# Optimization experiments

Measured on AMD Instinct MI355X. Metric: run time of the kernel, lower is better.

## Reference

```python
import jax, jax.numpy as jnp
import numpy as np

NUM_HEADS = 16
LORA_RANK = 64
LORA_ALPHA = 1.0


def setup_inputs() -> dict:
    key = jax.random.key(0)
    ks = jax.random.split(key, 9)
    B, N, C, r = 16, 1024, 1024, LORA_RANK
    s = lambda k, shp, sc=0.02: (jax.random.normal(k, shp, dtype=jnp.float32) * sc)
    return {
        "x": jax.random.normal(ks[0], (B, N, C), dtype=jnp.float32),
        "W_qkv": s(ks[1], (3 * C, C)),
        "b_qkv": s(ks[2], (3 * C,)),
        "lora_kA": s(ks[3], (r, C), 1.0 / np.sqrt(r)),
        "lora_kB": s(ks[4], (C, r)),
        "lora_vA": s(ks[5], (r, C), 1.0 / np.sqrt(r)),
        "lora_vB": s(ks[6], (C, r)),
        "W_proj": s(ks[7], (C, C)),
        "b_proj": s(ks[8], (C,)),
    }


def reference(x, W_qkv, b_qkv, lora_kA, lora_kB, lora_vA, lora_vB, W_proj, b_proj):
    B, N, C = x.shape
    H = NUM_HEADS
    D = C // H
    scale = D ** -0.5
    lora_scale = LORA_ALPHA / LORA_RANK

    # qkv projection: (B,N,3C)
    qkv = x @ W_qkv.T + b_qkv
    # LoRA deltas for k and v: x @ A.T @ B.T * (alpha/rank)
    k_lora = ((x @ lora_kA.T) @ lora_kB.T) * lora_scale  # (B,N,C)
    v_lora = ((x @ lora_vA.T) @ lora_vB.T) * lora_scale  # (B,N,C)

    qkv = qkv.reshape(B, N, 3, H, D).transpose(2, 0, 3, 1, 4)  # (3,B,H,N,D)
    q, k, v = qkv[0], qkv[1], qkv[2]
    k = k + k_lora.reshape(B, N, H, D).transpose(0, 2, 1, 3)
    v = v + v_lora.reshape(B, N, H, D).transpose(0, 2, 1, 3)

    attn = jnp.einsum('bhqd,bhkd->bhqk', q, k) * scale  # (B,H,N,N)
    attn = jax.nn.softmax(attn, axis=-1)
    out = jnp.einsum('bhqk,bhkd->bhqd', attn, v)  # (B,H,N,D)
    out = out.transpose(0, 2, 1, 3).reshape(B, N, C)
    return out @ W_proj.T + b_proj
```

## Files before the change

kernel.cpp:

```cpp
#include <hip/hip_runtime.h>
#include <hip/hip_bf16.h>
#include <stdint.h>

#define B_  16
#define N_  1024
#define C_  1024
#define H_  16
#define Dh  64
#define M_  (B_*N_)
#define QSCALE (0.125f * 1.44269504f)

typedef __attribute__((ext_vector_type(8)))  short short8;
typedef __attribute__((ext_vector_type(4)))  float f32x4;
typedef __attribute__((ext_vector_type(16))) float f32x16;

__device__ __forceinline__ ushort f2bf(float f) {
  union { float f; uint32_t u; } v; v.f = f;
  uint32_t u = v.u;
  u += 0x7fffu + ((u >> 16) & 1u);
  return (ushort)(u >> 16);
}

__device__ __forceinline__ float exp2fast(float x) {
#if __has_builtin(__builtin_amdgcn_exp2f)
  return __builtin_amdgcn_exp2f(x);
#else
  return exp2f(x);
#endif
}

__device__ __forceinline__ uint32_t pkbf(float lo, float hi) {
  float2 f; f.x = lo; f.y = hi;
  union { __hip_bfloat162 b; uint32_t u; } c;
  c.b = __float22bfloat162_rn(f);
  return c.u;
}

__device__ __forceinline__ void gload_lds16(const ushort* g, ushort* l) {
  __builtin_amdgcn_global_load_lds((const __attribute__((address_space(1))) void*)g,
                                   (__attribute__((address_space(3))) void*)l, 16, 0, 0);
}

struct CastSegs {
  const float* src[7];
  ushort*      dst[7];
  int          cum[7];
  float        scale[7];
};

__global__ void cast_all_k(CastSegs sg, int total4) {
  int i = blockIdx.x * blockDim.x + threadIdx.x;
  int stride = gridDim.x * blockDim.x;
  for (; i < total4; i += stride) {
    int s = 0;
    #pragma unroll
    for (int k = 0; k < 6; ++k) s += (i >= sg.cum[k]);
    int base = s ? sg.cum[s-1] : 0;
    int li = i - base;
    float sc = sg.scale[s];
    float4 v = reinterpret_cast<const float4*>(sg.src[s])[li];
    ushort4 o;
    o.x = f2bf(v.x * sc);
    o.y = f2bf(v.y * sc);
    o.z = f2bf(v.z * sc);
    o.w = f2bf(v.w * sc);
    reinterpret_cast<ushort4*>(sg.dst[s])[li] = o;
  }
}

template<int MODE>
__global__ __launch_bounds__(256)
void gemm128(const ushort* __restrict__ A, int lda,
             const ushort* __restrict__ Bm, int ldb,
             const float* __restrict__ bias,
             const ushort* __restrict__ A2,
             const ushort* __restrict__ B2k, const ushort* __restrict__ B2v,
             ushort* __restrict__ oq, ushort* __restrict__ ok, ushort* __restrict__ ov,
             float* __restrict__ of, int ldo)
{
  __shared__ ushort sA[2][128*32];
  __shared__ ushort sB[2][128*32];
  const int t = threadIdx.x;
  const int lane = t & 63, w = t >> 6;
  const int wr = w >> 1, wc = w & 1;
  const int r = lane & 15, g = lane >> 4;
  const int m0 = blockIdx.x * 128, n0 = blockIdx.y * 128;

  const int s = n0 >> 10;
  int nt = 32;
  const ushort* A2b = nullptr; const ushort* B2 = nullptr; int n0loc = 0;
  if (MODE == 1 && s == 1) {
    nt = 34;
    A2b = A2;
    B2 = B2k;
    n0loc = n0 - 1024;
  }
  if (MODE == 3) nt = 34;

  auto stage = [&](int buf, int tt) {
    const ushort* Ab; const ushort* Bb; int ldaT, ldbT;
    if (tt < 32) { Ab = A + m0*lda + tt*32; ldaT = lda; Bb = Bm + n0*ldb + tt*32; ldbT = ldb; }
    else if (MODE == 3) {
      Ab = A2 + m0*64 + (tt-32)*32; ldaT = 64;
      Bb = B2k + n0*128 + (tt-32)*32; ldbT = 128;
    } else {
      Ab = A2b + m0*128 + (tt-32)*32; ldaT = 128;
      Bb = B2 + n0loc*64 + (tt-32)*32; ldbT = 64;
    }
    #pragma unroll
    for (int i = 0; i < 2; ++i) {
      int c = i*256 + t;
      gload_lds16(Ab + (c>>2)*ldaT + (c&3)*8, &sA[buf][c*8]);
      gload_lds16(Bb + (c>>2)*ldbT + (c&3)*8, &sB[buf][c*8]);
    }
  };

  f32x4 acc[4][4];
  #pragma unroll
  for (int i=0;i<4;++i)
    #pragma unroll
    for (int j=0;j<4;++j) acc[i][j] = (f32x4){0.f,0.f,0.f,0.f};

  stage(0, 0);
  __syncthreads();
  for (int tt = 0; tt < nt; ++tt) {
    int cur = tt & 1;
    if (tt + 1 < nt) stage(cur ^ 1, tt + 1);
    short8 af[4], bfr[4];
    #pragma unroll
    for (int i=0;i<4;++i) af[i]  = *(const short8*)&sA[cur][(wr*64 + i*16 + r)*32 + g*8];
    #pragma unroll
    for (int j=0;j<4;++j) bfr[j] = *(const short8*)&sB[cur][(wc*64 + j*16 + r)*32 + g*8];
    #pragma unroll
    for (int i=0;i<4;++i)
      #pragma unroll
      for (int j=0;j<4;++j)
        acc[i][j] = __builtin_amdgcn_mfma_f32_16x16x32_bf16(af[i], bfr[j], acc[i][j], 0,0,0);
    __syncthreads();
  }

  #pragma unroll
  for (int i=0;i<4;++i) {
    #pragma unroll
    for (int j=0;j<4;++j) {
      #pragma unroll
      for (int rr=0;rr<4;++rr) {
        int m = m0 + wr*64 + i*16 + g*4 + rr;
        int n = n0 + wc*64 + j*16 + r;
        float v = acc[i][j][rr];
        if (MODE == 0) {
          oq[m*128 + n] = f2bf(v);
        } else if (MODE == 1) {
          v += bias[n];
          int b = m >> 10, nq = m & 1023;
          int c = n & 1023, h = c >> 6, d = c & 63;
          int idx = ((b*H_ + h)*N_ + nq)*Dh + d;
          if (s == 0)      oq[idx] = f2bf(v * QSCALE);
          else             ok[idx] = f2bf(v);
        } else if (MODE == 3) {
          v += bias[m];
          int h = m >> 6, d = m & 63;
          int b = n >> 10, nq = n & 1023;
          ov[((b*H_ + h)*Dh + d)*N_ + nq] = f2bf(v);
        } else {
          of[m*ldo + n] = v + bias[n];
        }
      }
    }
  }
}

__global__ __launch_bounds__(256, 4)
void flash_attn32(const ushort* __restrict__ qb, const ushort* __restrict__ kb,
                  const ushort* __restrict__ vb, ushort* __restrict__ out)
{
  __shared__ ushort Kt[2][64*64];
  __shared__ ushort Vt[2][64*64];
  const int t = threadIdx.x, w = t >> 6, lane = t & 63;
  const int ql = lane & 31, hi = lane >> 5;

  int bid = (blockIdx.x & 7) * 256 + (blockIdx.x >> 3);
  const int bh = bid >> 3, qt = bid & 7;
  const int b = bh >> 4, h = bh & 15;
  const ushort* Q  = qb + bh * (N_*Dh);
  const ushort* K  = kb + bh * (N_*Dh);
  const ushort* VT = vb + bh * (Dh*N_);
  const int q0 = qt*128 + w*32;

  short8 qf[4];
  #pragma unroll
  for (int ds=0; ds<4; ++ds)
    qf[ds] = *(const short8*)&Q[(q0 + ql)*Dh + ds*16 + hi*8];

  f32x16 o0, o1;
  #pragma unroll
  for (int r=0;r<16;++r) { o0[r]=0.f; o1[r]=0.f; }
  float lsum = 0.f;

  const int srow = t >> 3, scc = (t & 7) ^ ((t >> 3) & 7);
  const ushort* Ksrc0 = K  + srow*Dh + scc*8;
  const ushort* Vsrc0 = VT + srow*N_ + scc*8;
  ushort* Kdst = &Kt[0][t*8];
  ushort* Vdst = &Vt[0][t*8];

  const int km = ql & 7;
  int off[4];
  #pragma unroll
  for (int i=0;i<4;++i) off[i] = ql*64 + (((i*2 + hi) ^ km) * 8);

  auto stage = [&](int buf, int kt) {
    const ushort* Kp = Ksrc0 + kt*(64*Dh);
    const ushort* Vp = Vsrc0 + kt*64;
    gload_lds16(Kp,          Kdst + buf*4096);
    gload_lds16(Kp + 32*Dh,  Kdst + buf*4096 + 2048);
    gload_lds16(Vp,          Vdst + buf*4096);
    gload_lds16(Vp + 32*N_,  Vdst + buf*4096 + 2048);
  };

  auto tile = [&](const int cur, const int kt) {
    asm volatile("s_waitcnt vmcnt(0)" ::: "memory");
    __builtin_amdgcn_sched_barrier(0);
    __builtin_amdgcn_s_barrier();
    if (kt < 15) stage(cur ^ 1, kt + 1);

    f32x16 s0, s1;
    #pragma unroll
    for (int r=0;r<16;++r) { s0[r]=0.f; s1[r]=0.f; }
    __builtin_amdgcn_s_setprio(1);
    #pragma unroll
    for (int ds=0; ds<4; ++ds) {
      short8 kfA = *(const short8*)&Kt[cur][off[ds]];
      short8 kfB = *(const short8*)&Kt[cur][off[ds] + 2048];
      s0 = __builtin_amdgcn_mfma_f32_32x32x16_bf16(kfA, qf[ds], s0, 0,0,0);
      s1 = __builtin_amdgcn_mfma_f32_32x32x16_bf16(kfB, qf[ds], s1, 0,0,0);
    }
    __builtin_amdgcn_s_setprio(0);

    #pragma unroll
    for (int sg=0; sg<4; ++sg) {
      const int rb = (sg & 1) * 8;
      float e0,e1,e2,e3,e4,e5,e6,e7;
      if (sg < 2) {
        e0=exp2fast(s0[rb+0]); e1=exp2fast(s0[rb+1]);
        e2=exp2fast(s0[rb+2]); e3=exp2fast(s0[rb+3]);
        e4=exp2fast(s0[rb+4]); e5=exp2fast(s0[rb+5]);
        e6=exp2fast(s0[rb+6]); e7=exp2fast(s0[rb+7]);
      } else {
        e0=exp2fast(s1[rb+0]); e1=exp2fast(s1[rb+1]);
        e2=exp2fast(s1[rb+2]); e3=exp2fast(s1[rb+3]);
        e4=exp2fast(s1[rb+4]); e5=exp2fast(s1[rb+5]);
        e6=exp2fast(s1[rb+6]); e7=exp2fast(s1[rb+7]);
      }
      lsum += ((e0+e1)+(e2+e3)) + ((e4+e5)+(e6+e7));
      uint32_t w01 = pkbf(e0, e1);
      uint32_t w23 = pkbf(e2, e3);
      uint32_t w45 = pkbf(e4, e5);
      uint32_t w67 = pkbf(e6, e7);
      uint32_t t0 = hi ? w01 : w45;
      uint32_t t1 = hi ? w23 : w67;
      uint32_t xt0 = __shfl_xor(t0, 32);
      uint32_t xt1 = __shfl_xor(t1, 32);
      union { uint32_t u[4]; short8 s8; } pu;
      pu.u[0] = hi ? xt0 : w01;
      pu.u[1] = hi ? xt1 : w23;
      pu.u[2] = hi ? w45 : xt0;
      pu.u[3] = hi ? w67 : xt1;
      short8 pf = pu.s8;

      short8 vfA = *(const short8*)&Vt[cur][off[sg]];
      short8 vfB = *(const short8*)&Vt[cur][off[sg] + 2048];
      __builtin_amdgcn_s_setprio(1);
      o0 = __builtin_amdgcn_mfma_f32_32x32x16_bf16(pf, vfA, o0, 0,0,0);
      o1 = __builtin_amdgcn_mfma_f32_32x32x16_bf16(pf, vfB, o1, 0,0,0);
      __builtin_amdgcn_s_setprio(0);
    }
  };

  stage(0, 0);
  for (int ktp = 0; ktp < 16; ktp += 2) {
    tile(0, ktp);
    tile(1, ktp + 1);
  }

  float lfull = lsum + __shfl_xor(lsum, 32);
  float inv = 1.f / lfull;
  #pragma unroll
  for (int r=0;r<16;++r) {
    int qr = (r&3) + 8*(r>>2) + 4*hi;
    float invr = __shfl(inv, qr);
    int row = b*N_ + q0 + qr;
    out[row*C_ + h*Dh + ql]      = f2bf(o0[r] * invr);
    out[row*C_ + h*Dh + 32 + ql] = f2bf(o1[r] * invr);
  }
}

extern "C" void kernel_launch(void* const* d_in, const int* in_sizes, int n_in,
                              void* d_out, int out_size, void* d_ws, size_t ws_size,
                              hipStream_t stream)
{
  const float* x      = (const float*)d_in[0];
  const float* W_qkv  = (const float*)d_in[1];
  const float* b_qkv  = (const float*)d_in[2];
  const float* kA     = (const float*)d_in[3];
  const float* kB     = (const float*)d_in[4];
  const float* vA     = (const float*)d_in[5];
  const float* vB     = (const float*)d_in[6];
  const float* W_proj = (const float*)d_in[7];
  const float* b_proj = (const float*)d_in[8];
  float* out = (float*)d_out;

  ushort* ws    = (ushort*)d_ws;
  ushort* xb    = ws;
  ushort* wqkvb = xb + 16777216;
  ushort* kvAb  = wqkvb + 3145728;
  ushort* kBb   = kvAb + 131072;
  ushort* vBb   = kBb + 65536;
  ushort* wprojb= vBb + 65536;
  ushort* tkv   = wprojb + 1048576;
  ushort* qbuf  = tkv + 2097152;
  ushort* kbuf  = qbuf + 16777216;
  ushort* vbuf  = kbuf + 16777216;
  ushort* attn  = xb;

  const float ls = 1.0f / 64.0f;

  CastSegs sg;
  const float* srcs[7] = { x, W_qkv, kA, vA, kB, vB, W_proj };
  ushort* dsts[7]      = { xb, wqkvb, kvAb, kvAb + 65536, kBb, vBb, wprojb };
  int     n4s[7]       = { 16777216/4, 3145728/4, 65536/4, 65536/4, 65536/4, 65536/4, 1048576/4 };
  float   scs[7]       = { 1.f, 1.f, 1.f, 1.f, ls, ls, 1.f };
  int cum = 0;
  for (int i = 0; i < 7; ++i) {
    sg.src[i] = srcs[i]; sg.dst[i] = dsts[i]; sg.scale[i] = scs[i];
    cum += n4s[i]; sg.cum[i] = cum;
  }
  cast_all_k<<<dim3(4096), dim3(256), 0, stream>>>(sg, cum);

  gemm128<0><<<dim3(128, 1), dim3(256), 0, stream>>>(
      xb, 1024, kvAb, 1024, nullptr, nullptr, nullptr, nullptr,
      tkv, nullptr, nullptr, nullptr, 0);

  gemm128<1><<<dim3(128, 16), dim3(256), 0, stream>>>(
      xb, 1024, wqkvb, 1024, b_qkv, tkv, kBb, nullptr,
      qbuf, kbuf, nullptr, nullptr, 0);

  gemm128<3><<<dim3(8, 128), dim3(256), 0, stream>>>(
      wqkvb + 2048*1024, 1024, xb, 1024, b_qkv + 2048, vBb, tkv + 64, nullptr,
      nullptr, nullptr, vbuf, nullptr, 0);

  flash_attn32<<<dim3(2048), dim3(256), 0, stream>>>(qbuf, kbuf, vbuf, attn);

  gemm128<2><<<dim3(128, 8), dim3(256), 0, stream>>>(
      attn, 1024, wprojb, 1024, b_proj, nullptr, nullptr, nullptr,
      nullptr, nullptr, nullptr, out, 1024);
}
```

Before: 348.2 us.

## Swizzle GEMM tile order for L2 reuse and compute softmax rowsum via MFMA

Result: no change. 344.6 us (-1.0%).

```diff
diff --git a/kernel.cpp b/kernel.cpp
--- a/kernel.cpp
+++ b/kernel.cpp
@@ -84,7 +84,18 @@
   const int lane = t & 63, w = t >> 6;
   const int wr = w >> 1, wc = w & 1;
   const int r = lane & 15, g = lane >> 4;
-  const int m0 = blockIdx.x * 128, n0 = blockIdx.y * 128;
+
+  int id = blockIdx.x, bx, by;
+  if (MODE == 1 || MODE == 2) {
+    int pw = id & 63, pm = pw & 15, pn = pw >> 4, P = id >> 6;
+    bx = (P & 7) * 16 + pm;
+    by = (P >> 3) * 4 + pn;
+  } else if (MODE == 3) {
+    bx = id & 7; by = id >> 3;
+  } else {
+    bx = id; by = 0;
+  }
+  const int m0 = bx * 128, n0 = by * 128;
 
   const int s = n0 >> 10;
   int nt = 32;
@@ -192,10 +203,13 @@
   for (int ds=0; ds<4; ++ds)
     qf[ds] = *(const short8*)&Q[(q0 + ql)*Dh + ds*16 + hi*8];
 
-  f32x16 o0, o1;
-  #pragma unroll
-  for (int r=0;r<16;++r) { o0[r]=0.f; o1[r]=0.f; }
-  float lsum = 0.f;
+  short8 ones;
+  #pragma unroll
+  for (int j=0;j<8;++j) ones[j] = (short)0x3F80;
+
+  f32x16 o0, o1, lacc;
+  #pragma unroll
+  for (int r=0;r<16;++r) { o0[r]=0.f; o1[r]=0.f; lacc[r]=0.f; }
 
   const int srow = t >> 3, scc = (t & 7) ^ ((t >> 3) & 7);
   const ushort* Ksrc0 = K  + srow*Dh + scc*8;
@@ -251,7 +265,6 @@
         e4=exp2fast(s1[rb+4]); e5=exp2fast(s1[rb+5]);
         e6=exp2fast(s1[rb+6]); e7=exp2fast(s1[rb+7]);
       }
-      lsum += ((e0+e1)+(e2+e3)) + ((e4+e5)+(e6+e7));
       uint32_t w01 = pkbf(e0, e1);
       uint32_t w23 = pkbf(e2, e3);
       uint32_t w45 = pkbf(e4, e5);
@@ -270,8 +283,9 @@
       short8 vfA = *(const short8*)&Vt[cur][off[sg]];
       short8 vfB = *(const short8*)&Vt[cur][off[sg] + 2048];
       __builtin_amdgcn_s_setprio(1);
-      o0 = __builtin_amdgcn_mfma_f32_32x32x16_bf16(pf, vfA, o0, 0,0,0);
-      o1 = __builtin_amdgcn_mfma_f32_32x32x16_bf16(pf, vfB, o1, 0,0,0);
+      o0   = __builtin_amdgcn_mfma_f32_32x32x16_bf16(pf, vfA, o0, 0,0,0);
+      o1   = __builtin_amdgcn_mfma_f32_32x32x16_bf16(pf, vfB, o1, 0,0,0);
+      lacc = __builtin_amdgcn_mfma_f32_32x32x16_bf16(pf, ones, lacc, 0,0,0);
       __builtin_amdgcn_s_setprio(0);
     }
   };
@@ -282,15 +296,13 @@
     tile(1, ktp + 1);
   }
 
-  float lfull = lsum + __shfl_xor(lsum, 32);
-  float inv = 1.f / lfull;
   #pragma unroll
   for (int r=0;r<16;++r) {
+    float inv = 1.f / lacc[r];
     int qr = (r&3) + 8*(r>>2) + 4*hi;
-    float invr = __shfl(inv, qr);
     int row = b*N_ + q0 + qr;
-    out[row*C_ + h*Dh + ql]      = f2bf(o0[r] * invr);
-    out[row*C_ + h*Dh + 32 + ql] = f2bf(o1[r] * invr);
+    out[row*C_ + h*Dh + ql]      = f2bf(o0[r] * inv);
+    out[row*C_ + h*Dh + 32 + ql] = f2bf(o1[r] * inv);
   }
 }
 
@@ -336,21 +348,21 @@
   }
   cast_all_k<<<dim3(4096), dim3(256), 0, stream>>>(sg, cum);
 
-  gemm128<0><<<dim3(128, 1), dim3(256), 0, stream>>>(
+  gemm128<0><<<dim3(128), dim3(256), 0, stream>>>(
       xb, 1024, kvAb, 1024, nullptr, nullptr, nullptr, nullptr,
       tkv, nullptr, nullptr, nullptr, 0);
 
-  gemm128<1><<<dim3(128, 16), dim3(256), 0, stream>>>(
+  gemm128<1><<<dim3(2048), dim3(256), 0, stream>>>(
       xb, 1024, wqkvb, 1024, b_qkv, tkv, kBb, nullptr,
       qbuf, kbuf, nullptr, nullptr, 0);
 
-  gemm128<3><<<dim3(8, 128), dim3(256), 0, stream>>>(
+  gemm128<3><<<dim3(1024), dim3(256), 0, stream>>>(
       wqkvb + 2048*1024, 1024, xb, 1024, b_qkv + 2048, vBb, tkv + 64, nullptr,
       nullptr, nullptr, vbuf, nullptr, 0);
 
   flash_attn32<<<dim3(2048), dim3(256), 0, stream>>>(qbuf, kbuf, vbuf, attn);
 
-  gemm128<2><<<dim3(128, 8), dim3(256), 0, stream>>>(
+  gemm128<2><<<dim3(1024), dim3(256), 0, stream>>>(
       attn, 1024, wprojb, 1024, b_proj, nullptr, nullptr, nullptr,
       nullptr, nullptr, nullptr, out, 1024);
 }
```
